# Optimization experiments

Hardware: AMD Instinct MI355X
Metric: run time of the kernel (lower is better)

The kernel has to match this reference:

```python
import jax, jax.numpy as jnp
import numpy as np

N = 100000
E = 3200000
IN_C, HID_C, OUT_C = 128, 64, 16
NEG_SLOPE = 0.2


def setup_inputs() -> dict:
    key = jax.random.key(0)
    ks = jax.random.split(key, 12)
    x = jax.random.normal(ks[0], (N, IN_C), dtype=jnp.float32)
    # edges with no self-loops (reference then appends one self-loop per node,
    # matching add_remaining_self_loops on a loop-free graph)
    src = jax.random.randint(ks[1], (E,), 0, N)
    off = jax.random.randint(ks[2], (E,), 1, N)
    dst = (src + off) % N
    edge_index = jnp.stack([src, dst]).astype(jnp.int64)
    W1 = jax.random.normal(ks[3], (IN_C, HID_C), jnp.float32) / np.sqrt(IN_C)
    a_src1 = jax.random.normal(ks[4], (HID_C,), jnp.float32) / np.sqrt(HID_C)
    a_dst1 = jax.random.normal(ks[5], (HID_C,), jnp.float32) / np.sqrt(HID_C)
    b1 = jnp.zeros((HID_C,), jnp.float32)
    W2 = jax.random.normal(ks[6], (HID_C, OUT_C), jnp.float32) / np.sqrt(HID_C)
    a_src2 = jax.random.normal(ks[7], (OUT_C,), jnp.float32) / np.sqrt(OUT_C)
    a_dst2 = jax.random.normal(ks[8], (OUT_C,), jnp.float32) / np.sqrt(OUT_C)
    b2 = jnp.zeros((OUT_C,), jnp.float32)
    return {"x": x, "edge_index": edge_index, "W1": W1, "a_src1": a_src1,
            "a_dst1": a_dst1, "b1": b1, "W2": W2, "a_src2": a_src2,
            "a_dst2": a_dst2, "b2": b2}


def gat_conv(x, src, dst, W, a_src, a_dst, b):
    # x: [N, Cin] -> h: [N, Cout]
    h = x @ W
    # per-node attention halves, then per-edge score e_ij = LeakyReLU(a_s[src]+a_d[dst])
    s = h @ a_src  # [N]
    d = h @ a_dst  # [N]
    e = jax.nn.leaky_relu(s[src] + d[dst], NEG_SLOPE)  # [E']
    # segment softmax over incoming edges of each destination node
    m = jax.ops.segment_max(e, dst, num_segments=N)
    m = jnp.where(jnp.isfinite(m), m, 0.0)
    p = jnp.exp(e - m[dst])
    z = jax.ops.segment_sum(p, dst, num_segments=N)
    coef = p / (z[dst] + 1e-16)  # [E']
    # scatter-aggregate messages h[src] weighted by attention
    out = jax.ops.segment_sum(coef[:, None] * h[src], dst, num_segments=N)
    return out + b


def reference(x, edge_index, W1, a_src1, a_dst1, b1, W2, a_src2, a_dst2, b2):
    # add_remaining_self_loops: input graph has no self-loops, so append all N
    loop = jnp.arange(N, dtype=edge_index.dtype)
    src = jnp.concatenate([edge_index[0], loop])
    dst = jnp.concatenate([edge_index[1], loop])
    h = gat_conv(x, src, dst, W1, a_src1, a_dst1, b1)
    h = jax.nn.relu(h)  # dropout is identity at eval
    h = gat_conv(h, src, dst, W2, a_src2, a_dst2, b2)
    return jax.nn.log_softmax(h, axis=1)
```

## Files before the change

kernel.cpp:

```cpp
#include <hip/hip_runtime.h>
#include <math.h>

#define NEG 0.2f

__device__ __forceinline__ float leaky(float x){ return x >= 0.f ? x : NEG*x; }

__device__ __forceinline__ unsigned short f2b(float f){
    unsigned u = __float_as_uint(f);
    unsigned r = u + 0x7fffu + ((u >> 16) & 1u);
    return (unsigned short)(r >> 16);
}

__global__ __launch_bounds__(256) void rg1(const float* __restrict__ x,
        const float* __restrict__ W1, const float* __restrict__ a_src,
        const float* __restrict__ a_dst, unsigned short* __restrict__ h1b,
        float* __restrict__ s1, float* __restrict__ d1, int N,
        const int* __restrict__ ei, int* __restrict__ cnt,
        int* __restrict__ rank, int E, int ET)
{
    __shared__ float wsh[128][64];
    const int tid = threadIdx.x;
    const int gG1 = (N + 63) >> 6;
    if ((int)blockIdx.x < gG1) {
        const int rowbase = blockIdx.x * 64;
        #pragma unroll
        for (int i = 0; i < 8; ++i){
            int g = tid + i*256;
            ((float4*)&wsh[0][0])[g] = ((const float4*)W1)[g];
        }
        __syncthreads();
        const int tx = tid & 15, ty = tid >> 4;
        const int r0 = rowbase + ty*4;
        const float4* xr0 = (const float4*)(x + (size_t)min(r0+0, N-1)*128);
        const float4* xr1 = (const float4*)(x + (size_t)min(r0+1, N-1)*128);
        const float4* xr2 = (const float4*)(x + (size_t)min(r0+2, N-1)*128);
        const float4* xr3 = (const float4*)(x + (size_t)min(r0+3, N-1)*128);
        float acc[4][4];
        #pragma unroll
        for (int j=0;j<4;++j){
            #pragma unroll
            for (int c=0;c<4;++c) acc[j][c]=0.f;
        }
        #pragma unroll 4
        for (int k4 = 0; k4 < 32; ++k4){
            float4 xv[4], wv[4];
            xv[0] = xr0[k4]; xv[1] = xr1[k4]; xv[2] = xr2[k4]; xv[3] = xr3[k4];
            #pragma unroll
            for (int i=0;i<4;++i) wv[i] = *(const float4*)&wsh[k4*4+i][tx*4];
            #pragma unroll
            for (int j=0;j<4;++j){
                float x0=xv[j].x, x1=xv[j].y, x2=xv[j].z, x3=xv[j].w;
                acc[j][0]=fmaf(x0,wv[0].x,acc[j][0]); acc[j][1]=fmaf(x0,wv[0].y,acc[j][1]);
                acc[j][2]=fmaf(x0,wv[0].z,acc[j][2]); acc[j][3]=fmaf(x0,wv[0].w,acc[j][3]);
                acc[j][0]=fmaf(x1,wv[1].x,acc[j][0]); acc[j][1]=fmaf(x1,wv[1].y,acc[j][1]);
                acc[j][2]=fmaf(x1,wv[1].z,acc[j][2]); acc[j][3]=fmaf(x1,wv[1].w,acc[j][3]);
                acc[j][0]=fmaf(x2,wv[2].x,acc[j][0]); acc[j][1]=fmaf(x2,wv[2].y,acc[j][1]);
                acc[j][2]=fmaf(x2,wv[2].z,acc[j][2]); acc[j][3]=fmaf(x2,wv[2].w,acc[j][3]);
                acc[j][0]=fmaf(x3,wv[3].x,acc[j][0]); acc[j][1]=fmaf(x3,wv[3].y,acc[j][1]);
                acc[j][2]=fmaf(x3,wv[3].z,acc[j][2]); acc[j][3]=fmaf(x3,wv[3].w,acc[j][3]);
            }
        }
        const float4 asv = *(const float4*)&a_src[tx*4];
        const float4 adv = *(const float4*)&a_dst[tx*4];
        #pragma unroll
        for (int j=0;j<4;++j){
            int r = rowbase + ty*4 + j;
            float sv = acc[j][0]*asv.x + acc[j][1]*asv.y + acc[j][2]*asv.z + acc[j][3]*asv.w;
            float dv = acc[j][0]*adv.x + acc[j][1]*adv.y + acc[j][2]*adv.z + acc[j][3]*adv.w;
            #pragma unroll
            for (int dd=8; dd>0; dd>>=1){ sv += __shfl_xor(sv, dd, 16); dv += __shfl_xor(dv, dd, 16); }
            if (r < N){
                uint2 pk;
                pk.x = (unsigned)f2b(acc[j][0]) | ((unsigned)f2b(acc[j][1]) << 16);
                pk.y = (unsigned)f2b(acc[j][2]) | ((unsigned)f2b(acc[j][3]) << 16);
                *(uint2*)&h1b[(size_t)r*64 + tx*4] = pk;
                if (tx == 0){ s1[r] = sv; d1[r] = dv; }
            }
        }
    }
    int i0 = (blockIdx.x*256 + tid)*4;
    if (i0 >= ET) return;
    int4 r4;
    if (i0 + 3 < E){
        int4 d4 = *(const int4*)(ei + E + i0);
        r4.x = atomicAdd(&cnt[d4.x], 1);
        r4.y = atomicAdd(&cnt[d4.y], 1);
        r4.z = atomicAdd(&cnt[d4.z], 1);
        r4.w = atomicAdd(&cnt[d4.w], 1);
    } else {
        #pragma unroll
        for (int u = 0; u < 4; ++u){
            int i = i0 + u;
            int dst = (i < E) ? ei[E + i] : (i - E);
            ((int*)&r4)[u] = atomicAdd(&cnt[dst], 1);
        }
    }
    *(int4*)(rank + i0) = r4;
}

__global__ void k_scan1(const int* __restrict__ cnt, int* __restrict__ bsum, int n){
    __shared__ int sh[256];
    int b = blockIdx.x, tid = threadIdx.x;
    int start = b*1024, s = 0;
    for (int i = tid; i < 1024; i += 256){ int idx = start+i; s += (idx<n)?cnt[idx]:0; }
    sh[tid]=s; __syncthreads();
    for (int d=128; d>0; d>>=1){ if (tid<d) sh[tid]+=sh[tid+d]; __syncthreads(); }
    if (tid==0) bsum[b]=sh[0];
}
__global__ void k_scan3(const int* __restrict__ cnt, const int* __restrict__ bsum,
                        int* __restrict__ rowptr, int n){
    __shared__ int sh[256];
    __shared__ int basesh;
    int b = blockIdx.x, tid = threadIdx.x;
    int pb = 0;
    for (int i = tid; i < b; i += 256) pb += bsum[i];
    sh[tid] = pb; __syncthreads();
    for (int d=128; d>0; d>>=1){ if (tid<d) sh[tid]+=sh[tid+d]; __syncthreads(); }
    if (tid==0) basesh = sh[0];
    __syncthreads();
    int base = basesh;
    __syncthreads();
    int i0 = b*1024 + tid*4;
    int v[4]; int local=0;
    #pragma unroll
    for (int k=0;k<4;k++){ int idx=i0+k; v[k]=(idx<n)?cnt[idx]:0; local+=v[k]; }
    sh[tid]=local; __syncthreads();
    for (int d=1; d<256; d<<=1){
        int t = (tid>=d)? sh[tid-d] : 0;
        __syncthreads();
        sh[tid] += t;
        __syncthreads();
    }
    int off = base + sh[tid] - local;
    #pragma unroll
    for (int k=0;k<4;k++){
        int idx = i0+k;
        if (idx < n){
            rowptr[idx]=off; off += v[k];
            if (idx==n-1) rowptr[n]=off;
        }
    }
}

__global__ void k_score(const int* __restrict__ ei, const int* __restrict__ rank,
                        const int* __restrict__ rowptr,
                        const float* __restrict__ s, const float* __restrict__ d,
                        int2* __restrict__ csrp, int E, int ET){
    int i = blockIdx.x*256 + threadIdx.x;
    if (i >= ET) return;
    int src = (i < E) ? ei[i]     : (i - E);
    int dst = (i < E) ? ei[E + i] : (i - E);
    float pv = expf(leaky(s[src] + d[dst]));
    csrp[rowptr[dst] + rank[i]] = make_int2(src, __float_as_int(pv));
}

__global__ __launch_bounds__(256) void a1(const int* __restrict__ rowptr,
        const int2* __restrict__ csrp, const unsigned short* __restrict__ h1b,
        const float* __restrict__ b1, float* __restrict__ out1, int N)
{
    int wid = threadIdx.x>>6, lane = threadIdx.x&63;
    int n = blockIdx.x*4 + wid;
    if (n >= N) return;
    int base = rowptr[n], end = rowptr[n+1];
    int es = lane >> 3, cg = lane & 7;
    float a0=0.f,a1v=0.f,a2v=0.f,a3=0.f,a4=0.f,a5=0.f,a6=0.f,a7=0.f;
    float z = 0.f;
    for (int k = base + es; k < end; k += 8){
        int2 cp = csrp[k];
        float pv = __int_as_float(cp.y);
        z += pv;
        uint4 hv = *(const uint4*)(h1b + (size_t)cp.x*64 + cg*8);
        a0 = fmaf(pv, __uint_as_float(hv.x << 16),          a0);
        a1v= fmaf(pv, __uint_as_float(hv.x & 0xffff0000u),  a1v);
        a2v= fmaf(pv, __uint_as_float(hv.y << 16),          a2v);
        a3 = fmaf(pv, __uint_as_float(hv.y & 0xffff0000u),  a3);
        a4 = fmaf(pv, __uint_as_float(hv.z << 16),          a4);
        a5 = fmaf(pv, __uint_as_float(hv.z & 0xffff0000u),  a5);
        a6 = fmaf(pv, __uint_as_float(hv.w << 16),          a6);
        a7 = fmaf(pv, __uint_as_float(hv.w & 0xffff0000u),  a7);
    }
    #pragma unroll
    for (int m = 8; m <= 32; m <<= 1){
        a0 += __shfl_xor(a0, m); a1v += __shfl_xor(a1v, m);
        a2v += __shfl_xor(a2v, m); a3 += __shfl_xor(a3, m);
        a4 += __shfl_xor(a4, m); a5 += __shfl_xor(a5, m);
        a6 += __shfl_xor(a6, m); a7 += __shfl_xor(a7, m);
        z  += __shfl_xor(z, m);
    }
    if (es == 0){
        float zi = 1.f/(z + 1e-16f);
        const float4 b0 = *(const float4*)(b1 + cg*8);
        const float4 b4 = *(const float4*)(b1 + cg*8 + 4);
        float4 o0 = make_float4(fmaxf(a0*zi + b0.x, 0.f), fmaxf(a1v*zi + b0.y, 0.f),
                                fmaxf(a2v*zi + b0.z, 0.f), fmaxf(a3*zi + b0.w, 0.f));
        float4 o4 = make_float4(fmaxf(a4*zi + b4.x, 0.f), fmaxf(a5*zi + b4.y, 0.f),
                                fmaxf(a6*zi + b4.z, 0.f), fmaxf(a7*zi + b4.w, 0.f));
        float* op = out1 + (size_t)n*64 + cg*8;
        *(float4*)op = o0;
        *(float4*)(op+4) = o4;
    }
}

__global__ __launch_bounds__(256) void g2(const float* __restrict__ xin,
        const float* __restrict__ W2, const float* __restrict__ a_src,
        const float* __restrict__ a_dst, unsigned short* __restrict__ h2b,
        float* __restrict__ s2, float* __restrict__ d2, int N)
{
    __shared__ float w[64*16];
    const int tid = threadIdx.x;
    for (int k = tid; k < 64*16/4; k += 256)
        ((float4*)w)[k] = ((const float4*)W2)[k];
    __syncthreads();
    int idx = blockIdx.x*256 + tid;
    int n = idx >> 4, c = idx & 15;
    if (n >= N) return;
    const float as = a_src[c], ad = a_dst[c];
    const float4* xr = (const float4*)(xin + (size_t)n*64);
    float acc = 0.f;
    #pragma unroll
    for (int i4 = 0; i4 < 16; ++i4) {
        float4 v = xr[i4];
        acc = fmaf(v.x, w[(i4*4+0)*16 + c], acc);
        acc = fmaf(v.y, w[(i4*4+1)*16 + c], acc);
        acc = fmaf(v.z, w[(i4*4+2)*16 + c], acc);
        acc = fmaf(v.w, w[(i4*4+3)*16 + c], acc);
    }
    h2b[(size_t)n*16 + c] = f2b(acc);
    float sv = acc*as, dv = acc*ad;
    #pragma unroll
    for (int dd = 8; dd > 0; dd >>= 1){ sv += __shfl_xor(sv, dd, 16); dv += __shfl_xor(dv, dd, 16); }
    if (c == 0) { s2[n] = sv; d2[n] = dv; }
}

__global__ __launch_bounds__(256) void a2(const int* __restrict__ rowptr,
        const int2* __restrict__ csrp, const unsigned short* __restrict__ h2b,
        const float* __restrict__ b2, float* __restrict__ out, int N)
{
    int wid = threadIdx.x>>6, lane = threadIdx.x&63;
    int n = blockIdx.x*4 + wid;
    if (n >= N) return;
    int base = rowptr[n], end = rowptr[n+1];
    int es = lane >> 1, cg = lane & 1;
    float a[8] = {0.f,0.f,0.f,0.f,0.f,0.f,0.f,0.f};
    float z = 0.f;
    for (int k = base + es; k < end; k += 32){
        int2 cp = csrp[k];
        float pv = __int_as_float(cp.y);
        z += pv;
        uint4 hv = *(const uint4*)(h2b + (size_t)cp.x*16 + cg*8);
        a[0] = fmaf(pv, __uint_as_float(hv.x << 16),          a[0]);
        a[1] = fmaf(pv, __uint_as_float(hv.x & 0xffff0000u),  a[1]);
        a[2] = fmaf(pv, __uint_as_float(hv.y << 16),          a[2]);
        a[3] = fmaf(pv, __uint_as_float(hv.y & 0xffff0000u),  a[3]);
        a[4] = fmaf(pv, __uint_as_float(hv.z << 16),          a[4]);
        a[5] = fmaf(pv, __uint_as_float(hv.z & 0xffff0000u),  a[5]);
        a[6] = fmaf(pv, __uint_as_float(hv.w << 16),          a[6]);
        a[7] = fmaf(pv, __uint_as_float(hv.w & 0xffff0000u),  a[7]);
    }
    #pragma unroll
    for (int m = 2; m <= 32; m <<= 1){
        #pragma unroll
        for (int j = 0; j < 8; ++j) a[j] += __shfl_xor(a[j], m);
        z += __shfl_xor(z, m);
    }
    float zi = 1.f/(z + 1e-16f);
    const float4 b0 = *(const float4*)(b2 + cg*8);
    const float4 b4 = *(const float4*)(b2 + cg*8 + 4);
    float o[8];
    o[0]=a[0]*zi+b0.x; o[1]=a[1]*zi+b0.y; o[2]=a[2]*zi+b0.z; o[3]=a[3]*zi+b0.w;
    o[4]=a[4]*zi+b4.x; o[5]=a[5]*zi+b4.y; o[6]=a[6]*zi+b4.z; o[7]=a[7]*zi+b4.w;
    float mx = o[0];
    #pragma unroll
    for (int j = 1; j < 8; ++j) mx = fmaxf(mx, o[j]);
    mx = fmaxf(mx, __shfl_xor(mx, 1));
    float sum = 0.f;
    #pragma unroll
    for (int j = 0; j < 8; ++j) sum += expf(o[j] - mx);
    sum += __shfl_xor(sum, 1);
    if (es == 0){
        float ls = logf(sum);
        float* op = out + (size_t)n*16 + cg*8;
        *(float4*)op     = make_float4(o[0]-mx-ls, o[1]-mx-ls, o[2]-mx-ls, o[3]-mx-ls);
        *(float4*)(op+4) = make_float4(o[4]-mx-ls, o[5]-mx-ls, o[6]-mx-ls, o[7]-mx-ls);
    }
}

extern "C" void kernel_launch(void* const* d_in, const int* in_sizes, int n_in,
                              void* d_out, int out_size, void* d_ws, size_t ws_size,
                              hipStream_t stream)
{
    const float* x      = (const float*)d_in[0];
    const int*   ei     = (const int*)d_in[1];
    const float* W1     = (const float*)d_in[2];
    const float* a_src1 = (const float*)d_in[3];
    const float* a_dst1 = (const float*)d_in[4];
    const float* b1     = (const float*)d_in[5];
    const float* W2     = (const float*)d_in[6];
    const float* a_src2 = (const float*)d_in[7];
    const float* a_dst2 = (const float*)d_in[8];
    const float* b2     = (const float*)d_in[9];
    float* out = (float*)d_out;
    const int N  = in_sizes[0] / 128;
    const int E  = in_sizes[1] / 2;
    const int ET = E + N;

    char* ptr = (char*)d_ws;
    auto alloc = [&](size_t bytes)->char* {
        char* r = ptr; ptr += (bytes + 255) & ~(size_t)255; return r;
    };
    unsigned short* h1b    = (unsigned short*)alloc((size_t)N*64*2);
    unsigned short* h2b    = (unsigned short*)alloc((size_t)N*16*2);
    float*          out1   = (float*)alloc((size_t)N*64*4);
    float*          s1     = (float*)alloc((size_t)N*4);
    float*          d1     = (float*)alloc((size_t)N*4);
    float*          s2     = (float*)alloc((size_t)N*4);
    float*          d2v    = (float*)alloc((size_t)N*4);
    int*            cnt    = (int*)alloc((size_t)N*4);
    int*            rowptr = (int*)alloc((size_t)(N+1)*4);
    int*            rank   = (int*)alloc((size_t)(ET+3)*4);
    int2*           csrp   = (int2*)alloc((size_t)ET*8);
    int*            bsum   = (int*)alloc(4096);

    const int gET  = (ET + 255)/256;
    const int gET4 = ((ET+3)/4 + 255)/256;
    const int nb1  = (N + 1023)/1024;
    const int nbN4 = (N + 3)/4;
    const int gN16 = ((size_t)N*16 + 255)/256;
    const int gG1  = (N + 63)/64;
    const int gRG1 = (gET4 > gG1) ? gET4 : gG1;

    hipMemsetAsync(cnt, 0, (size_t)N*4, stream);
    rg1<<<gRG1, 256, 0, stream>>>(x, W1, a_src1, a_dst1, h1b, s1, d1, N,
                                  ei, cnt, rank, E, ET);
    k_scan1<<<nb1, 256, 0, stream>>>(cnt, bsum, N);
    k_scan3<<<nb1, 256, 0, stream>>>(cnt, bsum, rowptr, N);

    k_score<<<gET, 256, 0, stream>>>(ei, rank, rowptr, s1, d1, csrp, E, ET);
    a1<<<nbN4, 256, 0, stream>>>(rowptr, csrp, h1b, b1, out1, N);

    g2<<<gN16, 256, 0, stream>>>(out1, W2, a_src2, a_dst2, h2b, s2, d2v, N);
    k_score<<<gET, 256, 0, stream>>>(ei, rank, rowptr, s2, d2v, csrp, E, ET);
    a2<<<nbN4, 256, 0, stream>>>(rowptr, csrp, h2b, b2, out, N);
}
```

Measured before the change: 416.0 us.

## Privatize destination counters per XCD with workgroup-scope atomics

Splits the in-degree counter array into one copy per XCD, chosen from the hardware XCC id register. Each edge now counts with a workgroup-scope atomic into its XCD's private copy and tags its rank with the XCD id. The scan kernels sum the eight copies and turn each copy into a per-XCD starting offset, which the score kernel uses to place edges in CSR order. The aim is to avoid device-wide coherent atomics across XCDs. The cost is an 8x larger memset, more scan reads, and hard-coded limits (N below 2^17, ranks below 2^24), plus a reliance on same-XCD L2 atomicity for workgroup scope.

```diff
diff --git a/kernel.cpp b/kernel.cpp
--- a/kernel.cpp
+++ b/kernel.cpp
@@ -2,6 +2,8 @@
 #include <math.h>
 
 #define NEG 0.2f
+#define XS 17
+#define NXCD 8
 
 __device__ __forceinline__ float leaky(float x){ return x >= 0.f ? x : NEG*x; }
 
@@ -11,11 +13,21 @@
     return (unsigned short)(r >> 16);
 }
 
+__device__ __forceinline__ int get_xcd(){
+    unsigned x;
+    asm volatile("s_getreg_b32 %0, hwreg(20, 0, 4)" : "=s"(x));
+    return (int)(x & 7u);
+}
+
+__device__ __forceinline__ int wg_atomic_inc(int* p){
+    return __hip_atomic_fetch_add(p, 1, __ATOMIC_RELAXED, __HIP_MEMORY_SCOPE_WORKGROUP);
+}
+
 __global__ __launch_bounds__(256) void rg1(const float* __restrict__ x,
         const float* __restrict__ W1, const float* __restrict__ a_src,
         const float* __restrict__ a_dst, unsigned short* __restrict__ h1b,
         float* __restrict__ s1, float* __restrict__ d1, int N,
-        const int* __restrict__ ei, int* __restrict__ cnt,
+        const int* __restrict__ ei, int* __restrict__ cnt8,
         int* __restrict__ rank, int E, int ET)
 {
     __shared__ float wsh[128][64];
@@ -80,34 +92,43 @@
     }
     int i0 = (blockIdx.x*256 + tid)*4;
     if (i0 >= ET) return;
+    const int xcd = get_xcd();
+    int* cbase = cnt8 + ((size_t)xcd << XS);
+    const int xtag = xcd << 24;
     int4 r4;
     if (i0 + 3 < E){
         int4 d4 = *(const int4*)(ei + E + i0);
-        r4.x = atomicAdd(&cnt[d4.x], 1);
-        r4.y = atomicAdd(&cnt[d4.y], 1);
-        r4.z = atomicAdd(&cnt[d4.z], 1);
-        r4.w = atomicAdd(&cnt[d4.w], 1);
+        r4.x = wg_atomic_inc(&cbase[d4.x]) | xtag;
+        r4.y = wg_atomic_inc(&cbase[d4.y]) | xtag;
+        r4.z = wg_atomic_inc(&cbase[d4.z]) | xtag;
+        r4.w = wg_atomic_inc(&cbase[d4.w]) | xtag;
     } else {
         #pragma unroll
         for (int u = 0; u < 4; ++u){
             int i = i0 + u;
             int dst = (i < E) ? ei[E + i] : (i - E);
-            ((int*)&r4)[u] = atomicAdd(&cnt[dst], 1);
+            ((int*)&r4)[u] = wg_atomic_inc(&cbase[dst]) | xtag;
         }
     }
     *(int4*)(rank + i0) = r4;
 }
 
-__global__ void k_scan1(const int* __restrict__ cnt, int* __restrict__ bsum, int n){
+__global__ void k_scan1(const int* __restrict__ cnt8, int* __restrict__ bsum, int n){
     __shared__ int sh[256];
     int b = blockIdx.x, tid = threadIdx.x;
     int start = b*1024, s = 0;
-    for (int i = tid; i < 1024; i += 256){ int idx = start+i; s += (idx<n)?cnt[idx]:0; }
+    for (int i = tid; i < 1024; i += 256){
+        int idx = start+i;
+        if (idx < n){
+            #pragma unroll
+            for (int xx = 0; xx < NXCD; ++xx) s += cnt8[((size_t)xx<<XS) + idx];
+        }
+    }
     sh[tid]=s; __syncthreads();
     for (int d=128; d>0; d>>=1){ if (tid<d) sh[tid]+=sh[tid+d]; __syncthreads(); }
     if (tid==0) bsum[b]=sh[0];
 }
-__global__ void k_scan3(const int* __restrict__ cnt, const int* __restrict__ bsum,
+__global__ void k_scan3(int* __restrict__ cnt8, const int* __restrict__ bsum,
                         int* __restrict__ rowptr, int n){
     __shared__ int sh[256];
     __shared__ int basesh;
@@ -121,9 +142,16 @@
     int base = basesh;
     __syncthreads();
     int i0 = b*1024 + tid*4;
-    int v[4]; int local=0;
-    #pragma unroll
-    for (int k=0;k<4;k++){ int idx=i0+k; v[k]=(idx<n)?cnt[idx]:0; local+=v[k]; }
+    int c[4][NXCD]; int v[4]; int local=0;
+    #pragma unroll
+    for (int k=0;k<4;k++){
+        int idx=i0+k; int t = 0;
+        if (idx < n){
+            #pragma unroll
+            for (int xx = 0; xx < NXCD; ++xx){ c[k][xx] = cnt8[((size_t)xx<<XS) + idx]; t += c[k][xx]; }
+        }
+        v[k] = t; local += t;
+    }
     sh[tid]=local; __syncthreads();
     for (int d=1; d<256; d<<=1){
         int t = (tid>=d)? sh[tid-d] : 0;
@@ -136,22 +164,33 @@
     for (int k=0;k<4;k++){
         int idx = i0+k;
         if (idx < n){
-            rowptr[idx]=off; off += v[k];
+            rowptr[idx]=off;
+            int run = off;
+            #pragma unroll
+            for (int xx = 0; xx < NXCD; ++xx){
+                int t = c[k][xx];
+                cnt8[((size_t)xx<<XS) + idx] = run;
+                run += t;
+            }
+            off += v[k];
             if (idx==n-1) rowptr[n]=off;
         }
     }
 }
 
 __global__ void k_score(const int* __restrict__ ei, const int* __restrict__ rank,
-                        const int* __restrict__ rowptr,
+                        const int* __restrict__ offs,
                         const float* __restrict__ s, const float* __restrict__ d,
                         int2* __restrict__ csrp, int E, int ET){
     int i = blockIdx.x*256 + threadIdx.x;
     if (i >= ET) return;
     int src = (i < E) ? ei[i]     : (i - E);
     int dst = (i < E) ? ei[E + i] : (i - E);
+    int rk = rank[i];
+    int xcd = ((unsigned)rk) >> 24;
+    int lr  = rk & 0xFFFFFF;
     float pv = expf(leaky(s[src] + d[dst]));
-    csrp[rowptr[dst] + rank[i]] = make_int2(src, __float_as_int(pv));
+    csrp[offs[((size_t)xcd<<XS) + dst] + lr] = make_int2(src, __float_as_int(pv));
 }
 
 __global__ __launch_bounds__(256) void a1(const int* __restrict__ rowptr,
@@ -315,7 +354,7 @@
     float*          d1     = (float*)alloc((size_t)N*4);
     float*          s2     = (float*)alloc((size_t)N*4);
     float*          d2v    = (float*)alloc((size_t)N*4);
-    int*            cnt    = (int*)alloc((size_t)N*4);
+    int*            cnt8   = (int*)alloc((size_t)NXCD*(1u<<XS)*4);
     int*            rowptr = (int*)alloc((size_t)(N+1)*4);
     int*            rank   = (int*)alloc((size_t)(ET+3)*4);
     int2*           csrp   = (int2*)alloc((size_t)ET*8);
@@ -329,16 +368,16 @@
     const int gG1  = (N + 63)/64;
     const int gRG1 = (gET4 > gG1) ? gET4 : gG1;
 
-    hipMemsetAsync(cnt, 0, (size_t)N*4, stream);
+    hipMemsetAsync(cnt8, 0, (size_t)NXCD*(1u<<XS)*4, stream);
     rg1<<<gRG1, 256, 0, stream>>>(x, W1, a_src1, a_dst1, h1b, s1, d1, N,
-                                  ei, cnt, rank, E, ET);
-    k_scan1<<<nb1, 256, 0, stream>>>(cnt, bsum, N);
-    k_scan3<<<nb1, 256, 0, stream>>>(cnt, bsum, rowptr, N);
-
-    k_score<<<gET, 256, 0, stream>>>(ei, rank, rowptr, s1, d1, csrp, E, ET);
+                                  ei, cnt8, rank, E, ET);
+    k_scan1<<<nb1, 256, 0, stream>>>(cnt8, bsum, N);
+    k_scan3<<<nb1, 256, 0, stream>>>(cnt8, bsum, rowptr, N);
+
+    k_score<<<gET, 256, 0, stream>>>(ei, rank, cnt8, s1, d1, csrp, E, ET);
     a1<<<nbN4, 256, 0, stream>>>(rowptr, csrp, h1b, b1, out1, N);
 
     g2<<<gN16, 256, 0, stream>>>(out1, W2, a_src2, a_dst2, h2b, s2, d2v, N);
-    k_score<<<gET, 256, 0, stream>>>(ei, rank, rowptr, s2, d2v, csrp, E, ET);
+    k_score<<<gET, 256, 0, stream>>>(ei, rank, cnt8, s2, d2v, csrp, E, ET);
     a2<<<nbN4, 256, 0, stream>>>(rowptr, csrp, h2b, b2, out, N);
 }
```

After: 434.8 us. 4.5% more time.

## Fuse layer-2 projection into layer-1 aggregation and recompute scores inline

Applied to the files above, without the earlier changes.

The layer-2 linear projection (W2), the bf16 h2 write and the s2/d2 attention halves are now computed in the epilogue of the layer-1 aggregation kernel. This removes the out1 intermediate buffer and the separate g2 kernel. The second k_score pass is also dropped, and a2 now computes exp(leaky(s2[src]+d2[dst])) per edge while gathering neighbours. The cost is an extra random s2 gather and an exp per edge in a2, plus more registers and shuffles in a1.

```diff
diff --git a/kernel.cpp b/kernel.cpp
--- a/kernel.cpp
+++ b/kernel.cpp
@@ -156,13 +156,22 @@
 
 __global__ __launch_bounds__(256) void a1(const int* __restrict__ rowptr,
         const int2* __restrict__ csrp, const unsigned short* __restrict__ h1b,
-        const float* __restrict__ b1, float* __restrict__ out1, int N)
+        const float* __restrict__ b1, const float* __restrict__ W2,
+        const float* __restrict__ as2, const float* __restrict__ ad2,
+        unsigned short* __restrict__ h2b, float* __restrict__ s2,
+        float* __restrict__ d2, int N)
 {
     int wid = threadIdx.x>>6, lane = threadIdx.x&63;
+    int es = lane >> 3, cg = lane & 7;
+    float2 w2r[8];
+    #pragma unroll
+    for (int j = 0; j < 8; ++j)
+        w2r[j] = *(const float2*)&W2[(cg*8 + j)*16 + es*2];
+    const float2 asv = *(const float2*)&as2[es*2];
+    const float2 adv = *(const float2*)&ad2[es*2];
     int n = blockIdx.x*4 + wid;
     if (n >= N) return;
     int base = rowptr[n], end = rowptr[n+1];
-    int es = lane >> 3, cg = lane & 7;
     float a0=0.f,a1v=0.f,a2v=0.f,a3=0.f,a4=0.f,a5=0.f,a6=0.f,a7=0.f;
     float z = 0.f;
     for (int k = base + es; k < end; k += 8){
@@ -187,53 +196,36 @@
         a6 += __shfl_xor(a6, m); a7 += __shfl_xor(a7, m);
         z  += __shfl_xor(z, m);
     }
-    if (es == 0){
-        float zi = 1.f/(z + 1e-16f);
-        const float4 b0 = *(const float4*)(b1 + cg*8);
-        const float4 b4 = *(const float4*)(b1 + cg*8 + 4);
-        float4 o0 = make_float4(fmaxf(a0*zi + b0.x, 0.f), fmaxf(a1v*zi + b0.y, 0.f),
-                                fmaxf(a2v*zi + b0.z, 0.f), fmaxf(a3*zi + b0.w, 0.f));
-        float4 o4 = make_float4(fmaxf(a4*zi + b4.x, 0.f), fmaxf(a5*zi + b4.y, 0.f),
-                                fmaxf(a6*zi + b4.z, 0.f), fmaxf(a7*zi + b4.w, 0.f));
-        float* op = out1 + (size_t)n*64 + cg*8;
-        *(float4*)op = o0;
-        *(float4*)(op+4) = o4;
-    }
-}
-
-__global__ __launch_bounds__(256) void g2(const float* __restrict__ xin,
-        const float* __restrict__ W2, const float* __restrict__ a_src,
-        const float* __restrict__ a_dst, unsigned short* __restrict__ h2b,
-        float* __restrict__ s2, float* __restrict__ d2, int N)
-{
-    __shared__ float w[64*16];
-    const int tid = threadIdx.x;
-    for (int k = tid; k < 64*16/4; k += 256)
-        ((float4*)w)[k] = ((const float4*)W2)[k];
-    __syncthreads();
-    int idx = blockIdx.x*256 + tid;
-    int n = idx >> 4, c = idx & 15;
-    if (n >= N) return;
-    const float as = a_src[c], ad = a_dst[c];
-    const float4* xr = (const float4*)(xin + (size_t)n*64);
-    float acc = 0.f;
-    #pragma unroll
-    for (int i4 = 0; i4 < 16; ++i4) {
-        float4 v = xr[i4];
-        acc = fmaf(v.x, w[(i4*4+0)*16 + c], acc);
-        acc = fmaf(v.y, w[(i4*4+1)*16 + c], acc);
-        acc = fmaf(v.z, w[(i4*4+2)*16 + c], acc);
-        acc = fmaf(v.w, w[(i4*4+3)*16 + c], acc);
-    }
-    h2b[(size_t)n*16 + c] = f2b(acc);
-    float sv = acc*as, dv = acc*ad;
-    #pragma unroll
-    for (int dd = 8; dd > 0; dd >>= 1){ sv += __shfl_xor(sv, dd, 16); dv += __shfl_xor(dv, dd, 16); }
-    if (c == 0) { s2[n] = sv; d2[n] = dv; }
+    float zi = 1.f/(z + 1e-16f);
+    const float4 b0 = *(const float4*)(b1 + cg*8);
+    const float4 b4 = *(const float4*)(b1 + cg*8 + 4);
+    float o[8];
+    o[0]=fmaxf(a0*zi + b0.x, 0.f); o[1]=fmaxf(a1v*zi + b0.y, 0.f);
+    o[2]=fmaxf(a2v*zi + b0.z, 0.f); o[3]=fmaxf(a3*zi + b0.w, 0.f);
+    o[4]=fmaxf(a4*zi + b4.x, 0.f); o[5]=fmaxf(a5*zi + b4.y, 0.f);
+    o[6]=fmaxf(a6*zi + b4.z, 0.f); o[7]=fmaxf(a7*zi + b4.w, 0.f);
+    float pc0 = 0.f, pc1 = 0.f;
+    #pragma unroll
+    for (int j = 0; j < 8; ++j){
+        pc0 = fmaf(o[j], w2r[j].x, pc0);
+        pc1 = fmaf(o[j], w2r[j].y, pc1);
+    }
+    #pragma unroll
+    for (int m = 1; m <= 4; m <<= 1){ pc0 += __shfl_xor(pc0, m); pc1 += __shfl_xor(pc1, m); }
+    float sp = pc0*asv.x + pc1*asv.y;
+    float dp = pc0*adv.x + pc1*adv.y;
+    #pragma unroll
+    for (int m = 8; m <= 32; m <<= 1){ sp += __shfl_xor(sp, m); dp += __shfl_xor(dp, m); }
+    if (cg == 0){
+        unsigned pk = (unsigned)f2b(pc0) | ((unsigned)f2b(pc1) << 16);
+        *(unsigned*)&h2b[(size_t)n*16 + es*2] = pk;
+        if (es == 0){ s2[n] = sp; d2[n] = dp; }
+    }
 }
 
 __global__ __launch_bounds__(256) void a2(const int* __restrict__ rowptr,
         const int2* __restrict__ csrp, const unsigned short* __restrict__ h2b,
+        const float* __restrict__ s2, const float* __restrict__ d2,
         const float* __restrict__ b2, float* __restrict__ out, int N)
 {
     int wid = threadIdx.x>>6, lane = threadIdx.x&63;
@@ -241,11 +233,12 @@
     if (n >= N) return;
     int base = rowptr[n], end = rowptr[n+1];
     int es = lane >> 1, cg = lane & 1;
+    float dn = d2[n];
     float a[8] = {0.f,0.f,0.f,0.f,0.f,0.f,0.f,0.f};
     float z = 0.f;
     for (int k = base + es; k < end; k += 32){
         int2 cp = csrp[k];
-        float pv = __int_as_float(cp.y);
+        float pv = expf(leaky(s2[cp.x] + dn));
         z += pv;
         uint4 hv = *(const uint4*)(h2b + (size_t)cp.x*16 + cg*8);
         a[0] = fmaf(pv, __uint_as_float(hv.x << 16),          a[0]);
@@ -310,7 +303,6 @@
     };
     unsigned short* h1b    = (unsigned short*)alloc((size_t)N*64*2);
     unsigned short* h2b    = (unsigned short*)alloc((size_t)N*16*2);
-    float*          out1   = (float*)alloc((size_t)N*64*4);
     float*          s1     = (float*)alloc((size_t)N*4);
     float*          d1     = (float*)alloc((size_t)N*4);
     float*          s2     = (float*)alloc((size_t)N*4);
@@ -325,7 +317,6 @@
     const int gET4 = ((ET+3)/4 + 255)/256;
     const int nb1  = (N + 1023)/1024;
     const int nbN4 = (N + 3)/4;
-    const int gN16 = ((size_t)N*16 + 255)/256;
     const int gG1  = (N + 63)/64;
     const int gRG1 = (gET4 > gG1) ? gET4 : gG1;
 
@@ -336,9 +327,8 @@
     k_scan3<<<nb1, 256, 0, stream>>>(cnt, bsum, rowptr, N);
 
     k_score<<<gET, 256, 0, stream>>>(ei, rank, rowptr, s1, d1, csrp, E, ET);
-    a1<<<nbN4, 256, 0, stream>>>(rowptr, csrp, h1b, b1, out1, N);
-
-    g2<<<gN16, 256, 0, stream>>>(out1, W2, a_src2, a_dst2, h2b, s2, d2v, N);
-    k_score<<<gET, 256, 0, stream>>>(ei, rank, rowptr, s2, d2v, csrp, E, ET);
-    a2<<<nbN4, 256, 0, stream>>>(rowptr, csrp, h2b, b2, out, N);
-}
+    a1<<<nbN4, 256, 0, stream>>>(rowptr, csrp, h1b, b1, W2, a_src2, a_dst2,
+                                 h2b, s2, d2v, N);
+
+    a2<<<nbN4, 256, 0, stream>>>(rowptr, csrp, h2b, s2, d2v, b2, out, N);
+}
```

New measurement: 422.3 us. No clear change (+1.5%).
